# Optimization experiments

Measured on AMD Instinct MI355X. Metric: run time of the kernel, lower is better.

The kernel has to match this reference:

```python
import jax, jax.numpy as jnp
import numpy as np

B, S, E = 4, 1024, 1024
H, DH = 16, 64
P = 64  # prompt length
MASKED_BIAS = -10000.0


def setup_inputs() -> dict:
    key = jax.random.key(0)
    ks = jax.random.split(key, 9)
    return {
        "hidden_states": jax.random.normal(ks[0], (B, S, E), jnp.float32),
        "promptKey": jax.random.normal(ks[1], (B, H, P, DH), jnp.float32),
        "promptValue": jax.random.normal(ks[2], (B, H, P, DH), jnp.float32),
        "textualKey": jax.random.normal(ks[3], (B, H, S, DH), jnp.float32),
        "textualValue": jax.random.normal(ks[4], (B, H, S, DH), jnp.float32),
        "promptMask": jnp.ones((B, 1, S, P), jnp.bool_),
        "c_attn_w": jax.random.normal(ks[5], (E, 3 * E), jnp.float32) * 0.02,
        "c_attn_b": jnp.zeros((3 * E,), jnp.float32),
        "c_proj_w": jax.random.normal(ks[6], (E, E), jnp.float32) * 0.02,
        "c_proj_b": jnp.zeros((E,), jnp.float32),
    }


def _split_heads(t):
    # [B, S, E] -> [B, H, S, DH]
    b, s, _ = t.shape
    return t.reshape(b, s, H, DH).transpose(0, 2, 1, 3)


def reference(hidden_states, promptKey, promptValue, textualKey, textualValue,
              promptMask, c_attn_w, c_attn_b, c_proj_w, c_proj_b):
    qkv = hidden_states @ c_attn_w + c_attn_b          # [B,S,3E]
    q, k, v = jnp.split(qkv, 3, axis=-1)
    q, k, v = _split_heads(q), _split_heads(k), _split_heads(v)  # [B,H,S,DH]

    # scores against prompt KV, textual KV, and elementwise self term
    promptW = jnp.einsum("bhsd,bhpd->bhsp", q, promptKey)       # [B,H,S,P]
    textW = jnp.einsum("bhsd,bhtd->bhst", q, textualKey)        # [B,H,S,S]
    selfW = jnp.sum(q * k, axis=-1, keepdims=True)              # [B,H,S,1]
    attn_weights = jnp.concatenate((promptW, textW, selfW), axis=-1)
    attn_weights = attn_weights / jnp.sqrt(jnp.float32(DH))

    # non-residual causal mask: bias[qlen-qlen:qlen, 1:klen+1] -> strictly lower tri
    causal = jnp.tri(S, S, -1, dtype=bool)                      # [S,S]
    self_mask = jnp.ones((S, 1), dtype=bool)
    causal_self = jnp.concatenate((causal, self_mask), axis=-1)[None, None]  # [1,1,S,S+1]
    full_mask = jnp.concatenate(
        (promptMask, jnp.broadcast_to(causal_self, (B, 1, S, S + 1))), axis=-1)
    attn_weights = jnp.where(full_mask, attn_weights, MASKED_BIAS)
    attn_weights = jax.nn.softmax(attn_weights, axis=-1)

    wSelf = attn_weights[..., -1:]                              # [B,H,S,1]
    wRest = attn_weights[..., :-1]                              # [B,H,S,P+S]
    valuePast = jnp.concatenate((promptValue, textualValue), axis=-2)  # [B,H,P+S,DH]
    attn_output = jnp.einsum("bhsk,bhkd->bhsd", wRest, valuePast) + wSelf * v

    # merge heads and output projection
    attn_output = attn_output.transpose(0, 2, 1, 3).reshape(B, S, E)
    return attn_output @ c_proj_w + c_proj_b
```

## Files before the change

kernel.cpp:

```cpp
#include <hip/hip_runtime.h>
#include <hip/hip_bf16.h>
#include <stdint.h>

#define H_ 16
#define DH_ 64
#define S_ 1024
#define B_ 4
#define E_ 1024
#define P_ 64
#define BH_ (B_ * H_)
#define KV_ (P_ + S_)
#define NT_ 17
#define TILE_ELEMS 4096

typedef __attribute__((ext_vector_type(8))) short short8;
typedef __attribute__((ext_vector_type(4))) float floatx4;

#define MFMA_BF16(a, b, c) __builtin_amdgcn_mfma_f32_16x16x32_bf16((a), (b), (c), 0, 0, 0)

__device__ __forceinline__ float bf2f(unsigned short u) {
    union { float f; uint32_t i; } x;
    x.i = ((uint32_t)u) << 16;
    return x.f;
}
__device__ __forceinline__ unsigned short f2bf(float f) {
    uint32_t i = __float_as_uint(f);
    uint32_t r = (i + 0x7fffu + ((i >> 16) & 1u)) >> 16;
    return (unsigned short)r;
}

__device__ __forceinline__ void gl_lds16(const void* g, void* l) {
    __builtin_amdgcn_global_load_lds(
        (const __attribute__((address_space(1))) uint32_t*)g,
        (__attribute__((address_space(3))) uint32_t*)l, 16, 0, 0);
}

#define BARRIER() asm volatile("s_barrier" ::: "memory")
#define WAIT_VM(n) asm volatile("s_waitcnt vmcnt(" #n ")" ::: "memory")

__global__ void prep(const float* __restrict__ hidden, const float* __restrict__ cw,
                     const float* __restrict__ pw, const float* __restrict__ pK,
                     const float* __restrict__ tK, const float* __restrict__ pV,
                     const float* __restrict__ tV, unsigned short* __restrict__ Ah,
                     unsigned short* __restrict__ Wt1, unsigned short* __restrict__ Wt2,
                     unsigned short* __restrict__ Kp, unsigned short* __restrict__ Vp) {
    __shared__ float t[32][33];
    int bid = blockIdx.x, tid = threadIdx.x;
    if (bid < 4096) {
        int i = bid * 256 + tid;
        float4 v = ((const float4*)hidden)[i];
        ushort4 o;
        o.x = f2bf(v.x); o.y = f2bf(v.y); o.z = f2bf(v.z); o.w = f2bf(v.w);
        ((ushort4*)Ah)[i] = o;
    } else if (bid < 8192) {
        const float* in; unsigned short* out; int R, C, bxx, byy;
        if (bid < 7168) { int i = bid - 4096; in = cw; out = Wt1; R = 1024; C = 3072; bxx = i % 96; byy = i / 96; }
        else            { int i = bid - 7168; in = pw; out = Wt2; R = 1024; C = 1024; bxx = i % 32; byy = i / 32; }
        int tx = tid & 31, ty = tid >> 5;
        int c0 = bxx * 32, r0 = byy * 32;
#pragma unroll
        for (int i = 0; i < 4; ++i)
            t[ty + i * 8][tx] = in[(size_t)(r0 + ty + i * 8) * C + c0 + tx];
        __syncthreads();
#pragma unroll
        for (int i = 0; i < 4; ++i)
            out[(size_t)(c0 + ty + i * 8) * R + r0 + tx] = f2bf(t[tx][ty + i * 8]);
    } else {
        int gid0 = (bid - 8192) * 256 + tid;
        int half = gid0 / (BH_ * 8704);
        int gid = gid0 % (BH_ * 8704);
        int bh = gid / 8704, rem = gid % 8704;
        int tt = rem / 512, r2 = rem % 512;
        int f = r2 >> 6, lane = r2 & 63;
        int nt = f >> 1, h = f & 1, quad = lane >> 4, cl = lane & 15;
        unsigned short o[8];
        if (half == 0) {
            int key = tt * 64 + nt * 16 + cl;
            int dh = h * 32 + quad * 8;
            const float* src = (key < P_)
                ? pK + ((size_t)bh * P_ + key) * DH_ + dh
                : tK + ((size_t)bh * S_ + (key - P_)) * DH_ + dh;
#pragma unroll
            for (int u = 0; u < 8; ++u) o[u] = f2bf(src[u]);
            *(int4*)&Kp[(size_t)gid * 8] = *(int4*)o;
        } else {
            int dhn = nt * 16 + cl;
            int kbase = tt * 64 + h * 32 + quad * 8;
            const float* src = (kbase < P_)
                ? pV + ((size_t)bh * P_ + kbase) * DH_ + dhn
                : tV + ((size_t)bh * S_ + (kbase - P_)) * DH_ + dhn;
#pragma unroll
            for (int u = 0; u < 8; ++u) o[u] = f2bf(src[(size_t)u * DH_]);
            *(int4*)&Vp[(size_t)gid * 8] = *(int4*)o;
        }
    }
}

template <int MODE, int TM, int TN, int BK>
__global__ __launch_bounds__(256) void gemm_bt(
    const unsigned short* __restrict__ A, const unsigned short* __restrict__ Bt,
    const float* __restrict__ bias, float* __restrict__ Cout,
    unsigned short* __restrict__ Qo, unsigned short* __restrict__ Ko,
    unsigned short* __restrict__ Vo, int M, int N, int K) {
    constexpr int MI = TM / 32, NI = TN / 32;
    constexpr int NA = TM * BK / 2048;
    constexpr int NB = TN * BK / 2048;
    static_assert(NA + NB == 4, "vmcnt constant assumes 4 loads/tile");
    __shared__ __align__(16) unsigned short lA[2][TM * BK];
    __shared__ __align__(16) unsigned short lB[2][TN * BK];
    int tid = threadIdx.x;
    int wave = tid >> 6, lane = tid & 63, quad = lane >> 4, cl = lane & 15;
    int m0 = blockIdx.y * TM, n0 = blockIdx.x * TN;
    int wm = (wave >> 1) * (TM / 2), wn = (wave & 1) * (TN / 2);
    floatx4 acc[MI][NI];
#pragma unroll
    for (int mi = 0; mi < MI; ++mi)
#pragma unroll
        for (int ni = 0; ni < NI; ++ni) acc[mi][ni] = (floatx4){0.f, 0.f, 0.f, 0.f};

    auto issue = [&](int k0, int buf) {
#pragma unroll
        for (int li = 0; li < NA; ++li) {
            int o = (li * 256 + tid) * 16;
            int hh = o / (TM * 64), rr = (o % (TM * 64)) >> 6, c8 = (o >> 4) & 3;
            gl_lds16(A + (size_t)(m0 + rr) * K + k0 + hh * 32 + c8 * 8,
                     (char*)lA[buf] + o);
        }
#pragma unroll
        for (int li = 0; li < NB; ++li) {
            int o = (li * 256 + tid) * 16;
            int hh = o / (TN * 64), rr = (o % (TN * 64)) >> 6, c8 = (o >> 4) & 3;
            gl_lds16(Bt + (size_t)(n0 + rr) * K + k0 + hh * 32 + c8 * 8,
                     (char*)lB[buf] + o);
        }
    };
    auto compute = [&](int buf) {
#pragma unroll
        for (int kk = 0; kk < BK / 32; ++kk) {
            short8 af[MI], bfr[NI];
#pragma unroll
            for (int mi = 0; mi < MI; ++mi)
                af[mi] = *(const short8*)&lA[buf][kk * TM * 32 + (wm + mi * 16 + cl) * 32 + quad * 8];
#pragma unroll
            for (int ni = 0; ni < NI; ++ni)
                bfr[ni] = *(const short8*)&lB[buf][kk * TN * 32 + (wn + ni * 16 + cl) * 32 + quad * 8];
#pragma unroll
            for (int mi = 0; mi < MI; ++mi)
#pragma unroll
                for (int ni = 0; ni < NI; ++ni)
                    acc[mi][ni] = MFMA_BF16(af[mi], bfr[ni], acc[mi][ni]);
        }
    };

    int nT = K / BK;
    issue(0, 0);
    for (int t = 0; t < nT; ++t) {
        int buf = t & 1;
        if (t + 1 < nT) {
            issue((t + 1) * BK, buf ^ 1);
            WAIT_VM(4);
        } else {
            WAIT_VM(0);
        }
        BARRIER();
        compute(buf);
        BARRIER();
    }

#pragma unroll
    for (int ni = 0; ni < NI; ++ni) {
        int ncol = n0 + wn + ni * 16 + cl;
        float bv = bias[ncol];
#pragma unroll
        for (int mi = 0; mi < MI; ++mi) {
#pragma unroll
            for (int r = 0; r < 4; ++r) {
                int mrow = m0 + wm + mi * 16 + quad * 4 + r;
                float v = acc[mi][ni][r] + bv;
                if (MODE == 0) {
                    Cout[(size_t)mrow * N + ncol] = v;
                } else {
                    int which = ncol >> 10, e = ncol & 1023;
                    int hh = e >> 6, dh = e & 63;
                    int b = mrow >> 10, s = mrow & 1023;
                    size_t idx = ((size_t)(b * H_ + hh) * S_ + s) * DH_ + dh;
                    unsigned short* dst = (which == 0) ? Qo : ((which == 1) ? Ko : Vo);
                    dst[idx] = f2bf(v);
                }
            }
        }
    }
}

__global__ __launch_bounds__(256) void attn_k(
    const unsigned short* __restrict__ Q, const unsigned short* __restrict__ Kc,
    const unsigned short* __restrict__ Vc, const unsigned short* __restrict__ Kp,
    const unsigned short* __restrict__ Vp, unsigned short* __restrict__ Aout) {
    __shared__ __align__(16) unsigned short lK[TILE_ELEMS];
    __shared__ __align__(16) unsigned short lV[TILE_ELEMS];
    __shared__ __align__(16) unsigned short lP[4][16 * 72];
    int tid = threadIdx.x, wave = tid >> 6, lane = tid & 63;
    int quad = lane >> 4, cl = lane & 15;
    int l = blockIdx.x;
    int p = l >> 6, bh = l & 63;
    int b = bh >> 4, h = bh & 15;
    const unsigned short* Qb = Q + (size_t)bh * S_ * DH_;
    const unsigned short* Kb = Kc + (size_t)bh * S_ * DH_;
    const unsigned short* Vb = Vc + (size_t)bh * S_ * DH_;
    const unsigned short* Kpb = Kp + (size_t)bh * NT_ * TILE_ELEMS;
    const unsigned short* Vpb = Vp + (size_t)bh * NT_ * TILE_ELEMS;
    unsigned short* lp = lP[wave];
    int so = wave * 1024 + lane * 16;

    int x1 = p, x2 = 15 - p;
    int qb1 = x1 * 64 + wave * 16, qb2 = x2 * 64 + wave * 16;

    short8 a0_1 = *(const short8*)(Qb + (size_t)(qb1 + cl) * DH_ + quad * 8);
    short8 a1_1 = *(const short8*)(Qb + (size_t)(qb1 + cl) * DH_ + quad * 8 + 32);
    short8 a0_2 = *(const short8*)(Qb + (size_t)(qb2 + cl) * DH_ + quad * 8);
    short8 a1_2 = *(const short8*)(Qb + (size_t)(qb2 + cl) * DH_ + quad * 8 + 32);

    float lsum1[4] = {0.f, 0.f, 0.f, 0.f}, lsum2[4] = {0.f, 0.f, 0.f, 0.f};
    floatx4 O1[4], O2[4];
#pragma unroll
    for (int nt = 0; nt < 4; ++nt) {
        O1[nt] = (floatx4){0.f, 0.f, 0.f, 0.f};
        O2[nt] = (floatx4){0.f, 0.f, 0.f, 0.f};
    }

    int rl = wave * 16 + quad * 4;

    auto do_tile = [&](short8 a0, short8 a1, floatx4* O, float* lsum, bool diag) {
        floatx4 s[4];
#pragma unroll
        for (int nt = 0; nt < 4; ++nt) {
            s[nt] = (floatx4){0.f, 0.f, 0.f, 0.f};
            short8 k0 = *(const short8*)&lK[(nt * 2 + 0) * 512 + lane * 8];
            short8 k1 = *(const short8*)&lK[(nt * 2 + 1) * 512 + lane * 8];
            s[nt] = MFMA_BF16(a0, k0, s[nt]);
            s[nt] = MFMA_BF16(a1, k1, s[nt]);
        }
#pragma unroll
        for (int nt = 0; nt < 4; ++nt) {
            int col = nt * 16 + cl;
#pragma unroll
            for (int r = 0; r < 4; ++r) {
                float v = s[nt][r] * 0.125f;
                if (diag && col >= rl + r) v = -10000.0f;
                float pb = __expf(v);
                lsum[r] += pb;
                lp[(quad * 4 + r) * 72 + col] = f2bf(pb);
            }
        }
        asm volatile("s_waitcnt lgkmcnt(0)" ::: "memory");
        short8 p0 = *(const short8*)&lp[cl * 72 + quad * 8];
        short8 p1 = *(const short8*)&lp[cl * 72 + quad * 8 + 32];
#pragma unroll
        for (int nt = 0; nt < 4; ++nt) {
            short8 v0 = *(const short8*)&lV[(nt * 2 + 0) * 512 + lane * 8];
            short8 v1 = *(const short8*)&lV[(nt * 2 + 1) * 512 + lane * 8];
            O[nt] = MFMA_BF16(p0, v0, O[nt]);
            O[nt] = MFMA_BF16(p1, v1, O[nt]);
        }
    };

    int T1 = x1 + 2, Tu = x2 + 2;
    for (int t = 0; t < Tu; ++t) {
        __syncthreads();
        {
            const char* gK = (const char*)(Kpb + (size_t)t * TILE_ELEMS);
            const char* gV = (const char*)(Vpb + (size_t)t * TILE_ELEMS);
            gl_lds16(gK + so, (char*)lK + so);
            gl_lds16(gK + 4096 + so, (char*)lK + 4096 + so);
            gl_lds16(gV + so, (char*)lV + so);
            gl_lds16(gV + 4096 + so, (char*)lV + 4096 + so);
        }
        __syncthreads();

        do_tile(a0_2, a1_2, O2, lsum2, t == Tu - 1);
        if (t < T1) do_tile(a0_1, a1_1, O1, lsum1, t == T1 - 1);
    }

#pragma unroll
    for (int seg = 0; seg < 2; ++seg) {
        int qb = seg ? qb2 : qb1;
        float* lsum = seg ? lsum2 : lsum1;
        floatx4* O = seg ? O2 : O1;
#pragma unroll
        for (int r = 0; r < 4; ++r) {
            float rs = lsum[r];
            rs += __shfl_xor(rs, 1, 16);
            rs += __shfl_xor(rs, 2, 16);
            rs += __shfl_xor(rs, 4, 16);
            rs += __shfl_xor(rs, 8, 16);
            int row = qb + quad * 4 + r;
            const unsigned short* qp = Qb + (size_t)row * DH_ + cl * 4;
            const unsigned short* kp = Kb + (size_t)row * DH_ + cl * 4;
            float d = 0.f;
#pragma unroll
            for (int u = 0; u < 4; ++u) d += bf2f(qp[u]) * bf2f(kp[u]);
            d += __shfl_xor(d, 1, 16);
            d += __shfl_xor(d, 2, 16);
            d += __shfl_xor(d, 4, 16);
            d += __shfl_xor(d, 8, 16);
            float ps = __expf(d * 0.125f);
            float linv = 1.0f / (rs + ps);
#pragma unroll
            for (int nt = 0; nt < 4; ++nt) {
                float vv = bf2f(Vb[(size_t)row * DH_ + nt * 16 + cl]);
                float o = (O[nt][r] + ps * vv) * linv;
                Aout[((size_t)b * S_ + row) * E_ + h * DH_ + nt * 16 + cl] = f2bf(o);
            }
        }
    }
}

extern "C" void kernel_launch(void* const* d_in, const int* in_sizes, int n_in,
                              void* d_out, int out_size, void* d_ws, size_t ws_size,
                              hipStream_t stream) {
    const float* hidden = (const float*)d_in[0];
    const float* pK = (const float*)d_in[1];
    const float* pV = (const float*)d_in[2];
    const float* tK = (const float*)d_in[3];
    const float* tV = (const float*)d_in[4];
    const float* cw = (const float*)d_in[6];
    const float* cb = (const float*)d_in[7];
    const float* pw = (const float*)d_in[8];
    const float* pb = (const float*)d_in[9];
    float* out = (float*)d_out;

    unsigned short* ws = (unsigned short*)d_ws;
    unsigned short* Wt1 = ws;
    unsigned short* Wt2 = Wt1 + (size_t)3072 * 1024;
    unsigned short* Ah  = Wt2 + (size_t)1024 * 1024;
    unsigned short* Qw  = Ah + (size_t)4096 * 1024;
    unsigned short* Kw  = Qw + (size_t)BH_ * S_ * DH_;
    unsigned short* Vw  = Kw + (size_t)BH_ * S_ * DH_;
    unsigned short* Kp  = Vw + (size_t)BH_ * S_ * DH_;
    unsigned short* Vp  = Kp + (size_t)BH_ * NT_ * TILE_ELEMS;
    unsigned short* At  = Ah;

    prep<<<12544, 256, 0, stream>>>(hidden, cw, pw, pK, tK, pV, tV,
                                    Ah, Wt1, Wt2, Kp, Vp);
    gemm_bt<1, 128, 128, 32><<<dim3(3072 / 128, 4096 / 128), 256, 0, stream>>>(
        Ah, Wt1, cb, nullptr, Qw, Kw, Vw, 4096, 3072, 1024);
    attn_k<<<512, 256, 0, stream>>>(Qw, Kw, Vw, Kp, Vp, At);
    gemm_bt<0, 64, 64, 64><<<dim3(1024 / 64, 4096 / 128 * 2), 256, 0, stream>>>(
        At, Wt2, pb, out, nullptr, nullptr, nullptr, 4096, 1024, 1024);
}
```

Baseline: 198.6 us.

## Triple-buffer GEMM LDS loads and double-buffer attention KV tiles

The GEMM main loop moves from double to triple buffering, issuing loads two tiles ahead and waiting on vmcnt(8). The attention kernel now double-buffers K/V tiles in LDS and prefetches the next tile with async global-to-LDS loads before computing the current one, replacing the load-then-sync pattern. The goal is to hide global memory latency behind MFMA work. The cost is more LDS per block, which can reduce occupancy, and the attention LDS footprint doubles for K/V.

```diff
diff --git a/kernel.cpp b/kernel.cpp
--- a/kernel.cpp
+++ b/kernel.cpp
@@ -105,9 +105,9 @@
     constexpr int MI = TM / 32, NI = TN / 32;
     constexpr int NA = TM * BK / 2048;
     constexpr int NB = TN * BK / 2048;
-    static_assert(NA + NB == 4, "vmcnt constant assumes 4 loads/tile");
-    __shared__ __align__(16) unsigned short lA[2][TM * BK];
-    __shared__ __align__(16) unsigned short lB[2][TN * BK];
+    static_assert(NA + NB == 4, "vmcnt constants assume 4 loads/tile");
+    __shared__ __align__(16) unsigned short lA[3][TM * BK];
+    __shared__ __align__(16) unsigned short lB[3][TN * BK];
     int tid = threadIdx.x;
     int wave = tid >> 6, lane = tid & 63, quad = lane >> 4, cl = lane & 15;
     int m0 = blockIdx.y * TM, n0 = blockIdx.x * TN;
@@ -154,10 +154,13 @@
 
     int nT = K / BK;
     issue(0, 0);
+    issue(BK, 1);
     for (int t = 0; t < nT; ++t) {
-        int buf = t & 1;
-        if (t + 1 < nT) {
-            issue((t + 1) * BK, buf ^ 1);
+        int buf = t % 3;
+        if (t + 2 < nT) {
+            issue((t + 2) * BK, (t + 2) % 3);
+            WAIT_VM(8);
+        } else if (t + 1 < nT) {
             WAIT_VM(4);
         } else {
             WAIT_VM(0);
@@ -196,8 +199,8 @@
     const unsigned short* __restrict__ Q, const unsigned short* __restrict__ Kc,
     const unsigned short* __restrict__ Vc, const unsigned short* __restrict__ Kp,
     const unsigned short* __restrict__ Vp, unsigned short* __restrict__ Aout) {
-    __shared__ __align__(16) unsigned short lK[TILE_ELEMS];
-    __shared__ __align__(16) unsigned short lV[TILE_ELEMS];
+    __shared__ __align__(16) unsigned short lK[2][TILE_ELEMS];
+    __shared__ __align__(16) unsigned short lV[2][TILE_ELEMS];
     __shared__ __align__(16) unsigned short lP[4][16 * 72];
     int tid = threadIdx.x, wave = tid >> 6, lane = tid & 63;
     int quad = lane >> 4, cl = lane & 15;
@@ -230,13 +233,23 @@
 
     int rl = wave * 16 + quad * 4;
 
-    auto do_tile = [&](short8 a0, short8 a1, floatx4* O, float* lsum, bool diag) {
+    auto issue = [&](int t, int buf) {
+        const char* gK = (const char*)(Kpb + (size_t)t * TILE_ELEMS);
+        const char* gV = (const char*)(Vpb + (size_t)t * TILE_ELEMS);
+        gl_lds16(gK + so, (char*)lK[buf] + so);
+        gl_lds16(gK + 4096 + so, (char*)lK[buf] + 4096 + so);
+        gl_lds16(gV + so, (char*)lV[buf] + so);
+        gl_lds16(gV + 4096 + so, (char*)lV[buf] + 4096 + so);
+    };
+
+    auto do_tile = [&](int buf, short8 a0, short8 a1, floatx4* O, float* lsum,
+                       bool diag) {
         floatx4 s[4];
 #pragma unroll
         for (int nt = 0; nt < 4; ++nt) {
             s[nt] = (floatx4){0.f, 0.f, 0.f, 0.f};
-            short8 k0 = *(const short8*)&lK[(nt * 2 + 0) * 512 + lane * 8];
-            short8 k1 = *(const short8*)&lK[(nt * 2 + 1) * 512 + lane * 8];
+            short8 k0 = *(const short8*)&lK[buf][(nt * 2 + 0) * 512 + lane * 8];
+            short8 k1 = *(const short8*)&lK[buf][(nt * 2 + 1) * 512 + lane * 8];
             s[nt] = MFMA_BF16(a0, k0, s[nt]);
             s[nt] = MFMA_BF16(a1, k1, s[nt]);
         }
@@ -257,28 +270,29 @@
         short8 p1 = *(const short8*)&lp[cl * 72 + quad * 8 + 32];
 #pragma unroll
         for (int nt = 0; nt < 4; ++nt) {
-            short8 v0 = *(const short8*)&lV[(nt * 2 + 0) * 512 + lane * 8];
-            short8 v1 = *(const short8*)&lV[(nt * 2 + 1) * 512 + lane * 8];
+            short8 v0 = *(const short8*)&lV[buf][(nt * 2 + 0) * 512 + lane * 8];
+            short8 v1 = *(const short8*)&lV[buf][(nt * 2 + 1) * 512 + lane * 8];
             O[nt] = MFMA_BF16(p0, v0, O[nt]);
             O[nt] = MFMA_BF16(p1, v1, O[nt]);
         }
     };
 
     int T1 = x1 + 2, Tu = x2 + 2;
+    issue(0, 0);
     for (int t = 0; t < Tu; ++t) {
-        __syncthreads();
-        {
-            const char* gK = (const char*)(Kpb + (size_t)t * TILE_ELEMS);
-            const char* gV = (const char*)(Vpb + (size_t)t * TILE_ELEMS);
-            gl_lds16(gK + so, (char*)lK + so);
-            gl_lds16(gK + 4096 + so, (char*)lK + 4096 + so);
-            gl_lds16(gV + so, (char*)lV + so);
-            gl_lds16(gV + 4096 + so, (char*)lV + 4096 + so);
-        }
-        __syncthreads();
-
-        do_tile(a0_2, a1_2, O2, lsum2, t == Tu - 1);
-        if (t < T1) do_tile(a0_1, a1_1, O1, lsum1, t == T1 - 1);
+        int buf = t & 1;
+        if (t + 1 < Tu) {
+            issue(t + 1, buf ^ 1);
+            WAIT_VM(4);
+        } else {
+            WAIT_VM(0);
+        }
+        BARRIER();
+
+        do_tile(buf, a0_2, a1_2, O2, lsum2, t == Tu - 1);
+        if (t < T1) do_tile(buf, a0_1, a1_1, O1, lsum1, t == T1 - 1);
+
+        BARRIER();
     }
 
 #pragma unroll
```

Result: slower. 205.3 us (+3.4%).
